# Performance work log

Hardware: AMD Instinct MI355X
Metric: run time of the kernel (lower is better)

## Reference

```python
import jax, jax.numpy as jnp
from jax import lax
import numpy as np

B, T, N, C = 8, 12, 80, 12
HID, KS, KC = 32, 3, 2
OUT_HORIZON = 6
ALPHA = 3.0


def _xavier(key, shape):
    std = np.sqrt(2.0 / (shape[0] + shape[-1])).astype(np.float32)
    return jax.random.normal(key, shape, dtype=jnp.float32) * std


def setup_inputs():
    key = jax.random.key(0)
    ks = jax.random.split(key, 20)
    N2, C2 = N * N, C * C
    d_enc = (1 + HID) * KS * KC   # gates/candi input dim for encoder cell (input_dim=1)
    d_dec = (2 * HID) * KS * KC   # decoder cell input dim (output_dim=hidden)
    As = jax.random.uniform(ks[1], (N, N), dtype=jnp.float32)
    Ac = jax.random.uniform(ks[2], (C, C), dtype=jnp.float32)
    return dict(
        X_seq=jax.random.normal(ks[0], (B, T, N, C), dtype=jnp.float32),
        As=As / As.sum(-1, keepdims=True),   # row-stochastic graph for stable Chebyshev
        Ac=Ac / Ac.sum(-1, keepdims=True),
        WuS=_xavier(ks[3], (C, HID)), WvS=_xavier(ks[4], (C, HID)),
        WuC=_xavier(ks[5], (N, HID)), WvC=_xavier(ks[6], (N, HID)),
        WA_S=_xavier(ks[7], (N2, N2)), bA_S=jnp.zeros((N2,), jnp.float32),
        WP_S=_xavier(ks[8], (N2, N2)), bP_S=jnp.zeros((N2,), jnp.float32),
        WA_C=_xavier(ks[9], (C2, C2)), bA_C=jnp.zeros((C2,), jnp.float32),
        WP_C=_xavier(ks[10], (C2, C2)), bP_C=jnp.zeros((C2,), jnp.float32),
        enc_Wg=_xavier(ks[11], (d_enc, 2 * HID)), enc_bg=jnp.zeros((2 * HID,), jnp.float32),
        enc_Wc=_xavier(ks[12], (d_enc, HID)), enc_bc=jnp.zeros((HID,), jnp.float32),
        dec_Wg=_xavier(ks[13], (d_dec, 2 * HID)), dec_bg=jnp.zeros((2 * HID,), jnp.float32),
        dec_Wc=_xavier(ks[14], (d_dec, HID)), dec_bc=jnp.zeros((HID,), jnp.float32),
        W1=_xavier(ks[15], (HID, HID // 2)), b1=jnp.zeros((HID // 2,), jnp.float32),
        W2=_xavier(ks[16], (HID // 2, 1)), b2=jnp.zeros((1,), jnp.float32),
    )


def _mixed_fusion(A, P, WA, bA, WP, bP):
    n = A.shape[0]
    a = jax.nn.sigmoid(A.reshape(-1) @ WA + bA + P.reshape(-1) @ WP + bP).reshape(n, n)
    return a * A + (1.0 - a) * P


def _mgp(X, As, Ac, WuS, WvS, WuC, WvC, WA_S, bA_S, WP_S, bP_S, WA_C, bA_C, WP_C, bP_C):
    # X: [B,T,N,C]
    Us = jnp.tanh(ALPHA * (X @ WuS))           # [B,T,N,h]
    Vs = jnp.tanh(ALPHA * (X @ WvS))
    M = jnp.einsum('btnh,btmh->nm', Us, Vs)
    Ps = jax.nn.softmax(jax.nn.relu(M - M.T), axis=-1)
    Gs = _mixed_fusion(As, Ps, WA_S, bA_S, WP_S, bP_S)
    Xc = jnp.swapaxes(X, 2, 3)                 # [B,T,C,N]
    Uc = jnp.tanh(ALPHA * (Xc @ WuC))
    Vc = jnp.tanh(ALPHA * (Xc @ WvC))
    Mc = jnp.einsum('btnh,btmh->nm', Uc, Vc)
    Pc = jax.nn.softmax(jax.nn.relu(Mc - Mc.T), axis=-1)
    Gc = _mixed_fusion(Ac, Pc, WA_C, bA_C, WP_C, bP_C)
    return Gs, Gc


def _cheby(G, K):
    Gset = [jnp.eye(G.shape[0], dtype=G.dtype), G]
    for _ in range(2, K):
        Gset.append(2.0 * (G @ Gset[-1]) - Gset[-2])
    return Gset[:K]


def _bdg(X, Gs_set, Gc_set, W, b):
    # X: [B,N,C,D]; Chebyshev bidirectional diffusion: mode-1 then mode-2 products
    feats = []
    for Gn in Gs_set:
        Xn = jnp.einsum('bncl,nm->bmcl', X, Gn)
        for Gk in Gc_set:
            feats.append(jnp.einsum('bmcl,cd->bmdl', Xn, Gk))
    feat = jnp.concatenate(feats, axis=-1)     # [B,N,C,D*Ks*Kc]
    return jnp.einsum('bmdk,kh->bmdh', feat, W) + b


def _cell(Gs_set, Gc_set, Xt, H, Wg, bg, Wc, bc):
    XH = jnp.concatenate([Xt, H], axis=-1)
    g = _bdg(XH, Gs_set, Gc_set, Wg, bg)
    update = jax.nn.sigmoid(g[..., :HID])
    reset = jax.nn.sigmoid(g[..., HID:])
    cand = jnp.tanh(_bdg(jnp.concatenate([Xt, reset * H], axis=-1), Gs_set, Gc_set, Wc, bc))
    return (1.0 - update) * H + update * cand


def _forward(X_seq, As, Ac, WuS, WvS, WuC, WvC, WA_S, bA_S, WP_S, bP_S,
             WA_C, bA_C, WP_C, bP_C, enc_Wg, enc_bg, enc_Wc, enc_bc,
             dec_Wg, dec_bg, dec_Wc, dec_bc, W1, b1, W2, b2):
    Gs, Gc = _mgp(X_seq, As, Ac, WuS, WvS, WuC, WvC,
                  WA_S, bA_S, WP_S, bP_S, WA_C, bA_C, WP_C, bP_C)
    Gs_set = _cheby(Gs, KS)
    Gc_set = _cheby(Gc, KC)
    X5 = X_seq[..., None]                       # [B,T,N,C,1]

    def step(H, Xt):
        Hn = _cell(Gs_set, Gc_set, Xt, H, enc_Wg, enc_bg, enc_Wc, enc_bc)
        return Hn, None

    H0 = jnp.zeros((X_seq.shape[0], N, C, HID), dtype=X_seq.dtype)
    Hend, _ = lax.scan(step, H0, jnp.swapaxes(X5, 0, 1))  # scan over T

    # decoder: GRU cell fed with its own hidden, out_proj per step
    H_dec, Xin = Hend, Hend
    outs = []
    for _ in range(OUT_HORIZON):
        H_dec = _cell(Gs_set, Gc_set, Xin, H_dec, dec_Wg, dec_bg, dec_Wc, dec_bc)
        outs.append((jnp.tanh(0.0) + (H_dec @ W1 + b1)) @ W2 + b2)
        Xin = H_dec
    return jnp.stack(outs, axis=1)[..., 0]      # [B,out_horizon,N,C]


def reference(X_seq, As, Ac, WuS, WvS, WuC, WvC, WA_S, bA_S, WP_S, bP_S,
              WA_C, bA_C, WP_C, bP_C, enc_Wg, enc_bg, enc_Wc, enc_bc,
              dec_Wg, dec_bg, dec_Wc, dec_bc, W1, b1, W2, b2):
    return _forward(X_seq, As, Ac, WuS, WvS, WuC, WvC, WA_S, bA_S, WP_S, bP_S,
                    WA_C, bA_C, WP_C, bP_C, enc_Wg, enc_bg, enc_Wc, enc_bc,
                    dec_Wg, dec_bg, dec_Wc, dec_bc, W1, b1, W2, b2)
```

## Files before the change

### kernel.cpp

```cpp
#include <hip/hip_runtime.h>
#include <hip/hip_bf16.h>


__global__ void k_pack(const float* __restrict__ eWg, const float* __restrict__ eWc,
                       const float* __restrict__ dWg, const float* __restrict__ dWc,
                       const float* __restrict__ W1, const float* __restrict__ b1,
                       const float* __restrict__ W2, const float* __restrict__ b2,
                       float* encWgh, float* encWch, float* WgX, float* WcX,
                       float* decWgc, float* decWcx, float* decWch, float* w12, float* c0) {
  int t = threadIdx.x;
  for (int idx = t; idx < 192*64; idx += 256) {
    int row = idx / 64, hh = idx % 64; int f = row / 32, ll = row % 32;
    encWgh[idx] = eWg[(f*33 + 1 + ll)*64 + hh];
    decWgc[idx] = dWg[(f*64 + ll)*64 + hh] + dWg[(f*64 + 32 + ll)*64 + hh];
  }
  for (int idx = t; idx < 192*32; idx += 256) {
    int row = idx / 32, hh = idx % 32; int f = row / 32, ll = row % 32;
    encWch[idx] = eWc[(f*33 + 1 + ll)*32 + hh];
    decWcx[idx] = dWc[(f*64 + ll)*32 + hh];
    decWch[idx] = dWc[(f*64 + 32 + ll)*32 + hh];
  }
  for (int idx = t; idx < 384; idx += 256) { int f = idx/64, hh = idx%64; WgX[idx] = eWg[(f*33)*64 + hh]; }
  if (t < 192) { int f = t/32, hh = t%32; WcX[t] = eWc[(f*33)*32 + hh]; }
  if (t < 32) { float s = 0; for (int j = 0; j < 16; ++j) s += W1[t*16+j]*W2[j]; w12[t] = s; }
  if (t == 0) { float s = 0; for (int j = 0; j < 16; ++j) s += b1[j]*W2[j]; c0[0] = s + b2[0]; }
}

__global__ __launch_bounds__(256) void k_uv(const float* __restrict__ X,
                                            const float* __restrict__ WuS, const float* __restrict__ WvS,
                                            const float* __restrict__ WuC, const float* __restrict__ WvC,
                                            float* __restrict__ Us, float* __restrict__ Vs,
                                            float* __restrict__ Uc, float* __restrict__ Vc) {
  int t = threadIdx.x;
  int h = t & 31;
  if (blockIdx.x < 960) {
    int row = blockIdx.x*8 + (t >> 5);
    const float* xr = X + (size_t)row*12;
    float su = 0.f, sv = 0.f;
#pragma unroll
    for (int c = 0; c < 12; ++c) {
      float x = xr[c];
      su += x*WuS[c*32+h]; sv += x*WvS[c*32+h];
    }
    Us[(size_t)row*32 + h] = tanhf(3.f*su);
    Vs[(size_t)row*32 + h] = tanhf(3.f*sv);
  } else {
    int row = (blockIdx.x - 960)*8 + (t >> 5);
    int bt = row / 12, c = row % 12;
    const float* xb = X + (size_t)bt*960 + c;
    float su = 0.f, sv = 0.f;
    for (int n = 0; n < 80; ++n) {
      float x = xb[n*12];
      su += x*WuC[n*32+h]; sv += x*WvC[n*32+h];
    }
    Uc[(size_t)row*32 + h] = tanhf(3.f*su);
    Vc[(size_t)row*32 + h] = tanhf(3.f*sv);
  }
}

__global__ __launch_bounds__(256) void k_m_mc(const float* __restrict__ Us, const float* __restrict__ Vs,
                                              const float* __restrict__ Uc, const float* __restrict__ Vc,
                                              float* __restrict__ M, float* __restrict__ Mc) {
  __shared__ float su[8][16][33], sv[8][16][33];
  int t = threadIdx.x;
  if (blockIdx.x < 25) {
    int m0 = (blockIdx.x % 5)*16, n0 = (blockIdx.x / 5)*16;
    int tx = t & 15, ty = t >> 4;
    float acc = 0.f;
    for (int r0 = 0; r0 < 96; r0 += 8) {
      for (int idx = t; idx < 8*16*32; idx += 256) {
        int hh = idx & 31, i = (idx >> 5) & 15, rr = idx >> 9;
        su[rr][i][hh] = Us[((size_t)(r0+rr)*80 + n0 + i)*32 + hh];
        sv[rr][i][hh] = Vs[((size_t)(r0+rr)*80 + m0 + i)*32 + hh];
      }
      __syncthreads();
      for (int rr = 0; rr < 8; ++rr) {
#pragma unroll
        for (int hh = 0; hh < 32; ++hh) acc += su[rr][ty][hh] * sv[rr][tx][hh];
      }
      __syncthreads();
    }
    M[(n0+ty)*80 + (m0+tx)] = acc;
  } else {
    if (t < 144) {
      int c1 = t / 12, c2 = t % 12;
      float acc = 0.f;
      for (int r = 0; r < 96; ++r)
        for (int hh = 0; hh < 32; ++hh)
          acc += Uc[((size_t)r*12+c1)*32+hh] * Vc[((size_t)r*12+c2)*32+hh];
      Mc[t] = acc;
    }
  }
}

__global__ void k_softmax2(const float* __restrict__ Ms, float* __restrict__ Ps,
                           const float* __restrict__ Mc, float* __restrict__ Pc) {
  int lane = threadIdx.x;
  const float* M; float* P; int row, n;
  if (blockIdx.x < 80) { M = Ms; P = Ps; row = blockIdx.x; n = 80; }
  else                 { M = Mc; P = Pc; row = blockIdx.x - 80; n = 12; }
  float v0 = -1e30f, v1 = -1e30f;
  {
    int m = lane;
    if (m < n) { float a = M[row*n + m] - M[m*n + row]; v0 = a > 0.f ? a : 0.f; }
    m = 64 + lane;
    if (m < n) { float a = M[row*n + m] - M[m*n + row]; v1 = a > 0.f ? a : 0.f; }
  }
  float mx = fmaxf(v0, v1);
  for (int off = 32; off; off >>= 1) mx = fmaxf(mx, __shfl_xor(mx, off));
  float s = 0.f;
  if (lane < n)      { v0 = expf(v0 - mx); s += v0; }
  if (64 + lane < n) { v1 = expf(v1 - mx); s += v1; }
  for (int off = 32; off; off >>= 1) s += __shfl_xor(s, off);
  float inv = 1.f / s;
  if (lane < n)      P[row*n + lane] = v0 * inv;
  if (64 + lane < n) P[row*n + 64 + lane] = v1 * inv;
}

__global__ __launch_bounds__(256, 1) void k_fus_partial(
    const float* __restrict__ A, const float* __restrict__ P,
    const float* __restrict__ WA, const float* __restrict__ WP,
    float* __restrict__ part) {
  int lane = threadIdx.x, sub = threadIdx.y;
  int jb = (blockIdx.x + blockIdx.y) % 25;
  int chunk = blockIdx.y;
  int j = jb*256 + lane*4;
  int i0 = chunk*100 + sub*25;
  float4 acc = {0.f, 0.f, 0.f, 0.f};
#pragma unroll
  for (int ii = 0; ii < 25; ii += 5) {
    float a[5], p[5]; float4 wa[5], wp[5];
#pragma unroll
    for (int u = 0; u < 5; ++u) {
      int i = i0 + ii + u;
      a[u] = A[i]; p[u] = P[i];
      wa[u] = *(const float4*)(WA + (size_t)i*6400 + j);
      wp[u] = *(const float4*)(WP + (size_t)i*6400 + j);
    }
#pragma unroll
    for (int u = 0; u < 5; ++u) {
      acc.x += a[u]*wa[u].x + p[u]*wp[u].x;
      acc.y += a[u]*wa[u].y + p[u]*wp[u].y;
      acc.z += a[u]*wa[u].z + p[u]*wp[u].z;
      acc.w += a[u]*wa[u].w + p[u]*wp[u].w;
    }
  }
  __shared__ float4 red[4][64];
  red[sub][lane] = acc;
  __syncthreads();
  if (sub == 0) {
    float4 r0 = red[0][lane], r1 = red[1][lane], r2 = red[2][lane], r3 = red[3][lane];
    float4 o = {r0.x+r1.x+r2.x+r3.x, r0.y+r1.y+r2.y+r3.y,
                r0.z+r1.z+r2.z+r3.z, r0.w+r1.w+r2.w+r3.w};
    *(float4*)(part + (size_t)chunk*6400 + j) = o;
  }
}

__global__ void k_final2(const float* __restrict__ part,
                         const float* __restrict__ bA, const float* __restrict__ bP,
                         const float* __restrict__ A, const float* __restrict__ P,
                         float* __restrict__ G,
                         const float* __restrict__ Ac, const float* __restrict__ Pc,
                         const float* __restrict__ WA_C, const float* __restrict__ WP_C,
                         const float* __restrict__ bA_C, const float* __restrict__ bP_C,
                         float* __restrict__ Gc) {
  int t = threadIdx.x;
  if (blockIdx.x < 25) {
    int j = blockIdx.x*256 + t;
    float s = 0.f;
    for (int k = 0; k < 64; ++k) s += part[(size_t)k*6400 + j];
    s += bA[j] + bP[j];
    float a = 1.f / (1.f + expf(-s));
    G[j] = a*A[j] + (1.f - a)*P[j];
  } else if (t < 144) {
    float s = 0.f;
    for (int i = 0; i < 144; ++i) s += Ac[i]*WA_C[i*144+t] + Pc[i]*WP_C[i*144+t];
    s += bA_C[t] + bP_C[t];
    float a = 1.f / (1.f + expf(-s));
    Gc[t] = a*Ac[t] + (1.f - a)*Pc[t];
  }
}

__global__ void k_cheby(const float* __restrict__ G, float* __restrict__ G2) {
  int j = blockIdx.x*256 + threadIdx.x;
  int n = j / 80, m = j % 80;
  float s = 0.f;
  for (int k = 0; k < 80; ++k) s += G[n*80+k]*G[k*80+m];
  G2[j] = 2.f*s - (n == m ? 1.f : 0.f);
}

__global__ __launch_bounds__(256) void k_gx(const float* __restrict__ X,
                                            const float* __restrict__ Gs, const float* __restrict__ Gs2,
                                            const float* __restrict__ Gc,
                                            const float* __restrict__ WgX, const float* __restrict__ WcX,
                                            float* __restrict__ gXg, float* __restrict__ gXc,
                                            float* __restrict__ Hz) {
  int bt = blockIdx.x, q = blockIdx.y, t = threadIdx.x;
  for (int i = (bt*4 + q)*256 + t; i < 245760; i += 98304) Hz[i] = 0.f;
  __shared__ float xl[960], xg1[240], xg2[240], S[240*6];
  for (int i = t; i < 960; i += 256) xl[i] = X[(size_t)bt*960 + i];
  __syncthreads();
  if (t < 240) {
    int nl = t / 12, c = t % 12, n = q*20 + nl;
    float s1 = 0.f, s2 = 0.f;
    for (int np = 0; np < 80; ++np) { float x = xl[np*12 + c]; s1 += Gs[np*80+n]*x; s2 += Gs2[np*80+n]*x; }
    xg1[t] = s1; xg2[t] = s2;
    S[t*6+0] = xl[n*12+c]; S[t*6+2] = s1; S[t*6+4] = s2;
  }
  __syncthreads();
  if (t < 240) {
    int nl = t / 12, c = t % 12, n = q*20 + nl;
    float a1 = 0.f, a3 = 0.f, a5 = 0.f;
    for (int cp = 0; cp < 12; ++cp) {
      float g = Gc[cp*12 + c];
      a1 += xl[n*12+cp]*g; a3 += xg1[nl*12+cp]*g; a5 += xg2[nl*12+cp]*g;
    }
    S[t*6+1] = a1; S[t*6+3] = a3; S[t*6+5] = a5;
  }
  __syncthreads();
  for (int idx = t; idx < 240*64; idx += 256) {
    int h = idx % 64, pair = idx / 64; int nl = pair/12, c = pair%12; int n = q*20+nl;
    float s = 0.f;
#pragma unroll
    for (int f = 0; f < 6; ++f) s += S[pair*6+f] * WgX[f*64+h];
    gXg[((size_t)bt*960 + n*12 + c)*64 + h] = s;
  }
  for (int idx = t; idx < 240*32; idx += 256) {
    int h = idx % 32, pair = idx / 32; int nl = pair/12, c = pair%12; int n = q*20+nl;
    float s = 0.f;
#pragma unroll
    for (int f = 0; f < 6; ++f) s += S[pair*6+f] * WcX[f*32+h];
    gXc[((size_t)bt*960 + n*12 + c)*32 + h] = s;
  }
}

__global__ __launch_bounds__(256) void k_cell0(const float* __restrict__ gXg,
                                               const float* __restrict__ gXc,
                                               const float* __restrict__ ebg,
                                               const float* __restrict__ ebc,
                                               float* __restrict__ H) {
  int idx = blockIdx.x*256 + threadIdx.x;
  int b = idx / 30720, rem = idx % 30720;
  int pos = rem / 32, h = rem % 32;
  float gu = gXg[((size_t)(b*12)*960 + pos)*64 + h] + ebg[h];
  float gc = gXc[((size_t)(b*12)*960 + pos)*32 + h] + ebc[h];
  float u = 1.f / (1.f + expf(-gu));
  H[idx] = u * tanhf(gc);
}

template<int HOUT, int MODE, bool HAS_U2, bool HAS_FIELD, bool DO_PROJ>
__global__ __launch_bounds__(256) void k_cell(
    const float* __restrict__ U1, const float* __restrict__ W1p,
    const float* __restrict__ U2, const float* __restrict__ W2p,
    const float* __restrict__ field, int fbs,
    const float* __restrict__ bias,
    const float* __restrict__ Gsd, const float* __restrict__ Gs2d, const float* __restrict__ Gcd,
    const float* Hbuf, const float* updbuf,
    float* outA, float* outB,
    const float* __restrict__ w12p, const float* __restrict__ c0p,
    float* projp, int step)
{
  constexpr int MT = 2;
  constexpr int NG = 256 / HOUT;
  constexpr int NP = (MT*12) / NG;
  const int t = threadIdx.x;
  const int b = blockIdx.y;
  const int m0 = blockIdx.x * MT;
  __shared__ float fA[3*MT*384];
  __shared__ float fB[3*MT*384];
  __shared__ float Gcol[320];
  const int mg = t >> 7;
  const int u  = t & 127;
  const int c0 = u >> 5;
  const int l  = u & 31;
  const int h  = t % HOUT;
  const int pg = t / HOUT;
  int bofs[NP];
#pragma unroll
  for (int p = 0; p < NP; ++p) bofs[p] = (p*NG + pg) * 32;
  float outr[NP];
#pragma unroll
  for (int p = 0; p < NP; ++p) outr[p] = 0.f;

  for (int i = t; i < 320; i += 256) {
    int lev = i / 160, r = i % 160, mi = r / 80, n = r % 80;
    Gcol[i] = (lev ? Gs2d : Gsd)[n*80 + m0 + mi];
  }
  __syncthreads();

  const size_t ub_base = (size_t)b*80*12*32;
  const int nrounds = HAS_U2 ? 2 : 1;
  for (int rnd = 0; rnd < nrounds; ++rnd) {
    const float* U  = rnd ? U2 : U1;
    const float* Wp = rnd ? W2p : W1p;
    if (rnd) __syncthreads();
    float a0[3], a1[3], a2[3];
#pragma unroll
    for (int j = 0; j < 3; ++j) { a1[j] = 0.f; a2[j] = 0.f; }
    const float* Ub = U + ub_base;
    for (int n = 0; n < 80; ++n) {
      float g1 = Gcol[mg*80 + n];
      float g2 = Gcol[160 + mg*80 + n];
#pragma unroll
      for (int j = 0; j < 3; ++j) {
        float x = Ub[(n*12 + c0 + 4*j)*32 + l];
        a1[j] += g1*x; a2[j] += g2*x;
      }
    }
#pragma unroll
    for (int j = 0; j < 3; ++j) a0[j] = Ub[((m0+mg)*12 + c0 + 4*j)*32 + l];
#pragma unroll
    for (int j = 0; j < 3; ++j) {
      int cc = c0 + 4*j;
      fA[(0*MT+mg)*384 + cc*32 + l] = a0[j];
      fA[(1*MT+mg)*384 + cc*32 + l] = a1[j];
      fA[(2*MT+mg)*384 + cc*32 + l] = a2[j];
    }
    __syncthreads();
    for (int idx = t; idx < 3*MT*384; idx += 256) {
      int ll = idx & 31;
      int d  = (idx >> 5) % 12;
      int km = idx / 384;
      float s = 0.f;
#pragma unroll
      for (int c = 0; c < 12; ++c) s += fA[km*384 + c*32 + ll] * Gcd[c*12 + d];
      fB[km*384 + d*32 + ll] = s;
    }
    __syncthreads();
    for (int f = 0; f < 6; ++f) {
      int kn = f >> 1;
      const float* src = ((f & 1) ? fB : fA) + kn*MT*384;
#pragma unroll
      for (int l4 = 0; l4 < 8; ++l4) {
        const float w0 = Wp[(f*32 + l4*4 + 0)*HOUT + h];
        const float w1 = Wp[(f*32 + l4*4 + 1)*HOUT + h];
        const float w2 = Wp[(f*32 + l4*4 + 2)*HOUT + h];
        const float w3 = Wp[(f*32 + l4*4 + 3)*HOUT + h];
#pragma unroll
        for (int p = 0; p < NP; ++p) {
          const float4 v = *(const float4*)&src[bofs[p] + l4*4];
          outr[p] += v.x*w0 + v.y*w1 + v.z*w2 + v.w*w3;
        }
      }
    }
  }
#pragma unroll
  for (int p = 0; p < NP; ++p) {
    int pair = p*NG + pg;
    int m = pair / 12, c = pair % 12;
    int n = m0 + m;
    size_t oidx = (size_t)(b*80 + n)*12 + c;
    float g = outr[p] + bias[h];
    if (HAS_FIELD) g += field[(size_t)b*fbs + (size_t)(n*12 + c)*HOUT + h];
    if (MODE == 0) {
      float sg = 1.f / (1.f + expf(-g));
      size_t hb = oidx*32;
      if (h < 32) outA[hb + h] = sg;
      else        outB[hb + (h-32)] = sg * Hbuf[hb + (h-32)];
    } else {
      float cd = tanhf(g);
      size_t hi = oidx*32 + h;
      float uu = updbuf[hi];
      float hv = Hbuf[hi];
      float hn = (1.f - uu)*hv + uu*cd;
      outA[hi] = hn;
      if (DO_PROJ) {
        float pv = hn * w12p[h];
        for (int off = 16; off; off >>= 1) pv += __shfl_down(pv, off, 32);
        if (h == 0) projp[((size_t)(b*6 + step)*80 + n)*12 + c] = pv + c0p[0];
      }
    }
  }
}

extern "C" void kernel_launch(void* const* d_in, const int* in_sizes, int n_in,
                              void* d_out, int out_size, void* d_ws, size_t ws_size,
                              hipStream_t stream) {
  (void)in_sizes; (void)n_in; (void)out_size;
  const float* X    = (const float*)d_in[0];
  const float* As   = (const float*)d_in[1];
  const float* Ac   = (const float*)d_in[2];
  const float* WuS  = (const float*)d_in[3];
  const float* WvS  = (const float*)d_in[4];
  const float* WuC  = (const float*)d_in[5];
  const float* WvC  = (const float*)d_in[6];
  const float* WA_S = (const float*)d_in[7];
  const float* bA_S = (const float*)d_in[8];
  const float* WP_S = (const float*)d_in[9];
  const float* bP_S = (const float*)d_in[10];
  const float* WA_C = (const float*)d_in[11];
  const float* bA_C = (const float*)d_in[12];
  const float* WP_C = (const float*)d_in[13];
  const float* bP_C = (const float*)d_in[14];
  const float* eWg  = (const float*)d_in[15];
  const float* ebg  = (const float*)d_in[16];
  const float* eWc  = (const float*)d_in[17];
  const float* ebc  = (const float*)d_in[18];
  const float* dWg  = (const float*)d_in[19];
  const float* dbg  = (const float*)d_in[20];
  const float* dWc  = (const float*)d_in[21];
  const float* dbc  = (const float*)d_in[22];
  const float* W1   = (const float*)d_in[23];
  const float* b1   = (const float*)d_in[24];
  const float* W2   = (const float*)d_in[25];
  const float* b2   = (const float*)d_in[26];
  float* out = (float*)d_out;

  float* w = (float*)d_ws;
  size_t o = 0;
  auto alloc = [&](size_t n) { float* p = w + o; o += (n + 63) & ~(size_t)63; return p; };
  float* Us     = alloc(245760);
  float* Vs     = alloc(245760);
  float* Uc     = alloc(36864);
  float* Vc     = alloc(36864);
  float* Mb     = alloc(6400);
  float* Mc     = alloc(144);
  float* Ps     = alloc(6400);
  float* Pc     = alloc(144);
  float* part   = alloc((size_t)64*6400);
  float* Gs     = alloc(6400);
  float* Gc     = alloc(144);
  float* Gs2    = alloc(6400);
  float* encWgh = alloc(192*64);
  float* encWch = alloc(192*32);
  float* WgX    = alloc(384);
  float* WcX    = alloc(192);
  float* decWgc = alloc(192*64);
  float* decWcx = alloc(192*32);
  float* decWch = alloc(192*32);
  float* w12    = alloc(32);
  float* c0     = alloc(64);
  float* H      = alloc(245760);
  float* H2     = alloc(245760);
  float* upd    = alloc(245760);
  float* rH     = alloc(245760);
  float* gXg    = alloc((size_t)5898240);
  float* gXc    = alloc((size_t)2949120);
  if (o * sizeof(float) > ws_size) return;

  k_pack<<<1,256,0,stream>>>(eWg, eWc, dWg, dWc, W1, b1, W2, b2,
                             encWgh, encWch, WgX, WcX, decWgc, decWcx, decWch, w12, c0);
  k_uv<<<1104,256,0,stream>>>(X, WuS, WvS, WuC, WvC, Us, Vs, Uc, Vc);
  k_m_mc<<<26,256,0,stream>>>(Us, Vs, Uc, Vc, Mb, Mc);
  k_softmax2<<<92,64,0,stream>>>(Mb, Ps, Mc, Pc);
  k_fus_partial<<<dim3(25,64),dim3(64,4),0,stream>>>(As, Ps, WA_S, WP_S, part);
  k_final2<<<26,256,0,stream>>>(part, bA_S, bP_S, As, Ps, Gs,
                                Ac, Pc, WA_C, WP_C, bA_C, bP_C, Gc);
  k_cheby<<<25,256,0,stream>>>(Gs, Gs2);
  k_gx<<<dim3(96,4),256,0,stream>>>(X, Gs, Gs2, Gc, WgX, WcX, gXg, gXc, H);

  k_cell0<<<960,256,0,stream>>>(gXg, gXc, ebg, ebc, H);

  for (int t = 1; t < 12; ++t) {
    k_cell<64,0,false,true,false><<<dim3(40,8),256,0,stream>>>(
        H, encWgh, nullptr, nullptr, gXg + (size_t)t*61440, 737280, ebg,
        Gs, Gs2, Gc, H, nullptr, upd, rH, nullptr, nullptr, nullptr, 0);
    k_cell<32,1,false,true,false><<<dim3(40,8),256,0,stream>>>(
        rH, encWch, nullptr, nullptr, gXc + (size_t)t*30720, 368640, ebc,
        Gs, Gs2, Gc, H, upd, H, nullptr, nullptr, nullptr, nullptr, 0);
  }
  float* Hd = H; float* Hn = H2;
  for (int i = 0; i < 6; ++i) {
    k_cell<64,0,false,false,false><<<dim3(40,8),256,0,stream>>>(
        Hd, decWgc, nullptr, nullptr, nullptr, 0, dbg,
        Gs, Gs2, Gc, Hd, nullptr, upd, rH, nullptr, nullptr, nullptr, 0);
    k_cell<32,1,true,false,true><<<dim3(40,8),256,0,stream>>>(
        Hd, decWcx, rH, decWch, nullptr, 0, dbc,
        Gs, Gs2, Gc, Hd, upd, Hn, nullptr, w12, c0, out, i);
    float* tmp = Hd; Hd = Hn; Hn = tmp;
  }
}
```

Before: 979.0 us.

## Stage U tiles through double-buffered LDS in k_cell and fuse cell0 into k_gx

k_cell now copies the per-batch U slab into shared memory in 8-node chunks with float4 loads and double buffering, replacing the strided global reads in the graph-aggregation loop. The first encoder step (k_cell0) is folded into k_gx for blocks with t==0, which drops one launch and the H zero-fill. k_fus_partial loses its launch_bounds occupancy hint and its outer unroll. The chunk loop adds a barrier per chunk and 24KB of extra LDS per block, which may reduce occupancy.

```diff
diff --git a/kernel.cpp b/kernel.cpp
--- a/kernel.cpp
+++ b/kernel.cpp
@@ -117,7 +117,7 @@
   if (64 + lane < n) P[row*n + 64 + lane] = v1 * inv;
 }
 
-__global__ __launch_bounds__(256, 1) void k_fus_partial(
+__global__ __launch_bounds__(256) void k_fus_partial(
     const float* __restrict__ A, const float* __restrict__ P,
     const float* __restrict__ WA, const float* __restrict__ WP,
     float* __restrict__ part) {
@@ -127,7 +127,6 @@
   int j = jb*256 + lane*4;
   int i0 = chunk*100 + sub*25;
   float4 acc = {0.f, 0.f, 0.f, 0.f};
-#pragma unroll
   for (int ii = 0; ii < 25; ii += 5) {
     float a[5], p[5]; float4 wa[5], wp[5];
 #pragma unroll
@@ -193,10 +192,10 @@
                                             const float* __restrict__ Gs, const float* __restrict__ Gs2,
                                             const float* __restrict__ Gc,
                                             const float* __restrict__ WgX, const float* __restrict__ WcX,
+                                            const float* __restrict__ ebg, const float* __restrict__ ebc,
                                             float* __restrict__ gXg, float* __restrict__ gXc,
-                                            float* __restrict__ Hz) {
+                                            float* __restrict__ H) {
   int bt = blockIdx.x, q = blockIdx.y, t = threadIdx.x;
-  for (int i = (bt*4 + q)*256 + t; i < 245760; i += 98304) Hz[i] = 0.f;
   __shared__ float xl[960], xg1[240], xg2[240], S[240*6];
   for (int i = t; i < 960; i += 256) xl[i] = X[(size_t)bt*960 + i];
   __syncthreads();
@@ -232,20 +231,21 @@
     for (int f = 0; f < 6; ++f) s += S[pair*6+f] * WcX[f*32+h];
     gXc[((size_t)bt*960 + n*12 + c)*32 + h] = s;
   }
-}
-
-__global__ __launch_bounds__(256) void k_cell0(const float* __restrict__ gXg,
-                                               const float* __restrict__ gXc,
-                                               const float* __restrict__ ebg,
-                                               const float* __restrict__ ebc,
-                                               float* __restrict__ H) {
-  int idx = blockIdx.x*256 + threadIdx.x;
-  int b = idx / 30720, rem = idx % 30720;
-  int pos = rem / 32, h = rem % 32;
-  float gu = gXg[((size_t)(b*12)*960 + pos)*64 + h] + ebg[h];
-  float gc = gXc[((size_t)(b*12)*960 + pos)*32 + h] + ebc[h];
-  float u = 1.f / (1.f + expf(-gu));
-  H[idx] = u * tanhf(gc);
+  if (bt % 12 == 0) {
+    int b = bt / 12;
+    for (int idx = t; idx < 240*32; idx += 256) {
+      int h = idx & 31, pair = idx >> 5; int nl = pair/12, c = pair%12; int n = q*20+nl;
+      float sg = 0.f, sc = 0.f;
+#pragma unroll
+      for (int f = 0; f < 6; ++f) {
+        float sv = S[pair*6+f];
+        sg += sv*WgX[f*64+h];
+        sc += sv*WcX[f*32+h];
+      }
+      float uu = 1.f / (1.f + expf(-(sg + ebg[h])));
+      H[((size_t)(b*80) + n)*12*32 + (size_t)c*32 + h] = uu * tanhf(sc + ebc[h]);
+    }
+  }
 }
 
 template<int HOUT, int MODE, bool HAS_U2, bool HAS_FIELD, bool DO_PROJ>
@@ -269,6 +269,7 @@
   __shared__ float fA[3*MT*384];
   __shared__ float fB[3*MT*384];
   __shared__ float Gcol[320];
+  __shared__ float Ust[2][3072];
   const int mg = t >> 7;
   const int u  = t & 127;
   const int c0 = u >> 5;
@@ -286,25 +287,40 @@
     int lev = i / 160, r = i % 160, mi = r / 80, n = r % 80;
     Gcol[i] = (lev ? Gs2d : Gsd)[n*80 + m0 + mi];
   }
-  __syncthreads();
 
   const size_t ub_base = (size_t)b*80*12*32;
   const int nrounds = HAS_U2 ? 2 : 1;
   for (int rnd = 0; rnd < nrounds; ++rnd) {
     const float* U  = rnd ? U2 : U1;
     const float* Wp = rnd ? W2p : W1p;
+    const float* Ub = U + ub_base;
     if (rnd) __syncthreads();
+    {
+      const float4* s4 = (const float4*)Ub;
+      float4* d4 = (float4*)Ust[0];
+      d4[t] = s4[t]; d4[t+256] = s4[t+256]; d4[t+512] = s4[t+512];
+    }
     float a0[3], a1[3], a2[3];
 #pragma unroll
     for (int j = 0; j < 3; ++j) { a1[j] = 0.f; a2[j] = 0.f; }
-    const float* Ub = U + ub_base;
-    for (int n = 0; n < 80; ++n) {
-      float g1 = Gcol[mg*80 + n];
-      float g2 = Gcol[160 + mg*80 + n];
-#pragma unroll
-      for (int j = 0; j < 3; ++j) {
-        float x = Ub[(n*12 + c0 + 4*j)*32 + l];
-        a1[j] += g1*x; a2[j] += g2*x;
+    for (int ch = 0; ch < 10; ++ch) {
+      __syncthreads();
+      if (ch < 9) {
+        const float4* s4 = (const float4*)(Ub + (ch+1)*3072);
+        float4* d4 = (float4*)Ust[(ch+1) & 1];
+        d4[t] = s4[t]; d4[t+256] = s4[t+256]; d4[t+512] = s4[t+512];
+      }
+      const float* Uc_ = Ust[ch & 1];
+#pragma unroll
+      for (int n8 = 0; n8 < 8; ++n8) {
+        int n = ch*8 + n8;
+        float g1 = Gcol[mg*80 + n];
+        float g2 = Gcol[160 + mg*80 + n];
+#pragma unroll
+        for (int j = 0; j < 3; ++j) {
+          float x = Uc_[n8*384 + (c0 + 4*j)*32 + l];
+          a1[j] += g1*x; a2[j] += g2*x;
+        }
       }
     }
 #pragma unroll
@@ -447,9 +463,7 @@
   k_final2<<<26,256,0,stream>>>(part, bA_S, bP_S, As, Ps, Gs,
                                 Ac, Pc, WA_C, WP_C, bA_C, bP_C, Gc);
   k_cheby<<<25,256,0,stream>>>(Gs, Gs2);
-  k_gx<<<dim3(96,4),256,0,stream>>>(X, Gs, Gs2, Gc, WgX, WcX, gXg, gXc, H);
-
-  k_cell0<<<960,256,0,stream>>>(gXg, gXc, ebg, ebc, H);
+  k_gx<<<dim3(96,4),256,0,stream>>>(X, Gs, Gs2, Gc, WgX, WcX, ebg, ebc, gXg, gXc, H);
 
   for (int t = 1; t < 12; ++t) {
     k_cell<64,0,false,true,false><<<dim3(40,8),256,0,stream>>>(
```

New measurement: 1.013 ms. +3.5%, slower.
